# Kernel optimization log

Measured on AMD Instinct MI355X. Metric: run time of the kernel, lower is better.

The kernel has to match this reference:

```python
import jax, jax.numpy as jnp
import numpy as np

L = 2            # layer_num
NNEI = 120       # neighbors
ED = 64          # embed_dim
HD = 128         # hidden_dim
B = 4096         # nframes * nloc
SCALING = HD ** (-0.5)
LN_EPS = 1e-5


def _l2norm(x):
    # torch F.normalize: x / max(||x||, 1e-12)
    n = jnp.sqrt(jnp.sum(x * x, axis=-1, keepdims=True))
    return x / jnp.maximum(n, 1e-12)


def setup_inputs() -> dict:
    key = jax.random.key(0)
    ks = jax.random.split(key, 10)
    input_G = jax.random.normal(ks[0], (B, NNEI, ED), dtype=jnp.float32)
    nei_mask = jax.random.randint(ks[1], (B, NNEI), 0, 2) > 0
    nei_mask = nei_mask.at[:, 0].set(True)  # ensure >=1 valid neighbor (avoid all -inf rows)
    r = jax.random.normal(ks[2], (B, NNEI, 3), dtype=jnp.float32)
    input_r = _l2norm(r)  # normalized radial
    std_in = 1.0 / np.sqrt(3 * HD + ED)
    std_out = 1.0 / np.sqrt(ED + HD)
    in_w = jax.random.normal(ks[3], (L, ED, 3 * HD), dtype=jnp.float32) * std_in
    in_b = jax.random.normal(ks[4], (L, 3 * HD), dtype=jnp.float32)
    out_w = jax.random.normal(ks[5], (L, HD, ED), dtype=jnp.float32) * std_out
    out_b = jax.random.normal(ks[6], (L, ED), dtype=jnp.float32)
    ln_g = jnp.ones((L, ED), dtype=jnp.float32)
    ln_b = jnp.zeros((L, ED), dtype=jnp.float32)
    return {"input_G": input_G, "nei_mask": nei_mask, "input_r": input_r,
            "in_w": in_w, "in_b": in_b, "out_w": out_w, "out_b": out_b,
            "ln_g": ln_g, "ln_b": ln_b}


def _layer_norm(x, g, b):
    mu = jnp.mean(x, axis=-1, keepdims=True)
    var = jnp.mean((x - mu) ** 2, axis=-1, keepdims=True)
    return (x - mu) * jax.lax.rsqrt(var + LN_EPS) * g + b


def reference(input_G, nei_mask, input_r, in_w, in_b, out_w, out_b, ln_g, ln_b):
    # angular gate: [B, nnei, nnei]
    ang = jnp.einsum('bnd,bmd->bnm', input_r, input_r)
    mask_k = nei_mask[:, None, :]   # mask over keys
    mask_q = nei_mask[:, :, None]   # mask over queries
    x = input_G
    for l in range(L):
        residual = x
        qkv = jnp.einsum('bne,ef->bnf', x, in_w[l]) + in_b[l]
        q, k, v = jnp.split(qkv, 3, axis=-1)           # each [B, nnei, HD]
        q = _l2norm(q) * SCALING
        k = _l2norm(k)
        v = _l2norm(v)
        aw = jnp.einsum('bnh,bmh->bnm', q, k)
        aw = jnp.where(mask_k, aw, -jnp.inf)
        aw = jax.nn.softmax(aw, axis=-1)
        aw = jnp.where(mask_q, aw, 0.0)
        aw = aw * ang                                   # dotr angular gating
        o = jnp.einsum('bnm,bmh->bnh', aw, v)
        x = residual + jnp.einsum('bnh,he->bne', o, out_w[l]) + out_b[l]
        x = _layer_norm(x, ln_g[l], ln_b[l])            # post_ln
    return x
```

## Files before the change

kernel.cpp:

```cpp
#include <hip/hip_runtime.h>
#include <math.h>

#define LAYERS 2
#define NNEI 120
#define NPAD 128
#define ED 64
#define HD 128
#define NB 4096
#define F3 (3*HD)
#define SCALING 0.088388347648318447f
#define LN_EPS 1e-5f
#define T 512
#define XP 72
#define QPAD 136

typedef unsigned short u16;
typedef unsigned int u32;
typedef unsigned char u8;
typedef float f32x4 __attribute__((ext_vector_type(4)));
typedef short bf16x8 __attribute__((ext_vector_type(8)));

__device__ __forceinline__ float bf2f(u16 u) { return __uint_as_float(((u32)u) << 16); }
__device__ __forceinline__ u16 f2bf(float f) {
  u32 i = __float_as_uint(f);
  u32 r = (i + 0x7fffu + ((i >> 16) & 1u)) >> 16;
  return (u16)r;
}
__device__ __forceinline__ float gldr(const void* p, long i, bool f32) {
  return f32 ? ((const float*)p)[i] : bf2f(((const u16*)p)[i]);
}

__device__ __forceinline__ float red16sum(float v) {
  v += __shfl_xor(v, 1); v += __shfl_xor(v, 2);
  v += __shfl_xor(v, 4); v += __shfl_xor(v, 8);
  return v;
}
__device__ __forceinline__ float red16max(float v) {
  v = fmaxf(v, __shfl_xor(v, 1)); v = fmaxf(v, __shfl_xor(v, 2));
  v = fmaxf(v, __shfl_xor(v, 4)); v = fmaxf(v, __shfl_xor(v, 8));
  return v;
}

#define MFMA(a, b, d) (d) = __builtin_amdgcn_mfma_f32_16x16x32_bf16((a), (b), (d), 0, 0, 0)

__device__ __forceinline__ void gload_lds16(const u16* src, u16* dst) {
  __builtin_amdgcn_global_load_lds(
      (const __attribute__((address_space(1))) u32*)(const void*)src,
      (__attribute__((address_space(3))) u32*)(void*)dst, 16, 0, 0);
}

__device__ __forceinline__ void stage16(const u16* __restrict__ hi, const u16* __restrict__ lo,
                                        long base, int kstride, u16* sbuf, int wave, int lane) {
  #pragma unroll
  for (int kk = 0; kk < 2; ++kk) {
    const int i = 2 * wave + kk;
    const int col = 4 * i + (lane >> 4);
    const int slot = lane & 15;
    const int chunk = (slot & 7) ^ (col & 7);
    const u16* src = ((slot < 8) ? hi : lo) + base + (long)col * kstride + 8 * chunk;
    gload_lds16(src, sbuf + i * 512);
  }
}

__device__ __forceinline__ bf16x8 rdfrag(const u16* sbuf, int col, int chunk, int c7, int lo) {
  const int slot = (chunk ^ c7) + (lo << 3);
  return *(const bf16x8*)(sbuf + col * 128 + slot * 8);
}

__global__ void detect_kernel(const u16* __restrict__ G,
                              const u8* __restrict__ mask,
                              int* __restrict__ flags) {
  __shared__ int sf[2];
  const int t = threadIdx.x;
  if (t < 2) sf[t] = 0;
  __syncthreads();
  int isf = 0;
  for (int i = t; i < 256; i += 256) {
    int e = (G[2 * i] >> 7) & 0xff;
    if (e >= 150) isf = 1;
  }
  int mb = 0;
  for (int i = t; i < 4096; i += 256) {
    if (i && (i & 3) && mask[i]) mb = 1;
  }
  if (isf) atomicOr(&sf[0], 1);
  if (mb) atomicOr(&sf[1], 1);
  __syncthreads();
  if (t < 2) flags[t] = sf[t];
}

__global__ void prep_kernel(const void* __restrict__ in_w, const void* __restrict__ out_w,
                            u16* __restrict__ wt_hi, u16* __restrict__ wt_lo,
                            u16* __restrict__ ow_hi, u16* __restrict__ ow_lo,
                            const int* __restrict__ flags) {
  const bool f32 = flags[0] != 0;
  const int i = blockIdx.x * blockDim.x + threadIdx.x;
  if (i < LAYERS * F3 * ED) {
    const int l = i / (F3 * ED);
    const int rem = i % (F3 * ED);
    const int f = rem / ED;
    const int e = rem % ED;
    const long src = (long)(l * ED + e) * F3 + f;
    const float w = f32 ? ((const float*)in_w)[src] : bf2f(((const u16*)in_w)[src]);
    const u16 h = f2bf(w);
    wt_hi[i] = h;
    wt_lo[i] = f2bf(w - bf2f(h));
  }
  if (i < LAYERS * ED * HD) {
    const int l = i / (ED * HD);
    const int rem = i % (ED * HD);
    const int e = rem / HD;
    const int hh = rem % HD;
    const long src = (long)(l * HD + hh) * ED + e;
    const float w = f32 ? ((const float*)out_w)[src] : bf2f(((const u16*)out_w)[src]);
    const u16 h = f2bf(w);
    ow_hi[i] = h;
    ow_lo[i] = f2bf(w - bf2f(h));
  }
}

__global__ __launch_bounds__(T, 2) void nwa_kernel(
    const void* __restrict__ G, const void* __restrict__ mask,
    const void* __restrict__ rr,
    const void* __restrict__ in_b, const void* __restrict__ out_b,
    const void* __restrict__ ln_g, const void* __restrict__ ln_b,
    const u16* __restrict__ wt_hi, const u16* __restrict__ wt_lo,
    const u16* __restrict__ ow_hi, const u16* __restrict__ ow_lo,
    void* __restrict__ out, const int* __restrict__ flags)
{
  const bool f32f = flags[0] != 0;
  const bool mbyte = flags[1] != 0;

  __shared__ __align__(16) u16 x_hi[NPAD][XP];
  __shared__ __align__(16) u16 x_lo[NPAD][XP];
  __shared__ __align__(16) u16 q_s[NPAD][QPAD];
  __shared__ __align__(16) u16 k_s[NPAD][QPAD];
  __shared__ __align__(16) u16 vT_s[HD][QPAD];
  __shared__ __align__(16) float r_s[NPAD][4];
  __shared__ int m_s[NPAD];

  const int b = blockIdx.x;
  const int t = threadIdx.x;
  const int wave = t >> 6;
  const int lane = t & 63;
  const int g = lane >> 4;
  const int c = lane & 15;
  const int c7 = c & 7;
  u16* sbase = &q_s[0][0];

  {
    const long gbase = (long)b * (NNEI * ED);
    for (int i = t; i < NNEI * ED; i += T) {
      const int rrow = i >> 6, cc = i & 63;
      if (f32f) {
        const float v = ((const float*)G)[gbase + i];
        const u16 h = f2bf(v);
        x_hi[rrow][cc] = h;
        x_lo[rrow][cc] = f2bf(v - bf2f(h));
      } else {
        x_hi[rrow][cc] = ((const u16*)G)[gbase + i];
        x_lo[rrow][cc] = 0;
      }
    }
    for (int i = t; i < (NPAD - NNEI) * ED; i += T) {
      x_hi[NNEI + (i >> 6)][i & 63] = 0;
      x_lo[NNEI + (i >> 6)][i & 63] = 0;
    }
    const long rbase = (long)b * (NNEI * 3);
    const long mbase = (long)b * NNEI;
    for (int i = t; i < NPAD; i += T) {
      if (i < NNEI) {
        r_s[i][0] = gldr(rr, rbase + i * 3 + 0, f32f);
        r_s[i][1] = gldr(rr, rbase + i * 3 + 1, f32f);
        r_s[i][2] = gldr(rr, rbase + i * 3 + 2, f32f);
        r_s[i][3] = 0.f;
        m_s[i] = mbyte ? (int)((const u8*)mask)[mbase + i] : ((const int*)mask)[mbase + i];
      } else {
        r_s[i][0] = 0.f; r_s[i][1] = 0.f; r_s[i][2] = 0.f; r_s[i][3] = 0.f;
        m_s[i] = 0;
      }
    }
  }
  __syncthreads();

  int vmask = 0;
  #pragma unroll
  for (int mt = 0; mt < 8; ++mt) vmask |= (m_s[16 * mt + c] ? 1 : 0) << mt;
  float qmr[4];
  #pragma unroll
  for (int r = 0; r < 4; ++r) qmr[r] = m_s[16 * wave + 4 * g + r] ? 1.f : 0.f;

  for (int l = 0; l < LAYERS; ++l) {
    const long wofs = (long)l * (F3 * ED);
    const long bbase = (long)l * F3;
    const long oofs = (long)l * (ED * HD);

    bf16x8 a_hi[2], a_lo[2];
    #pragma unroll
    for (int kf = 0; kf < 2; ++kf) {
      a_hi[kf] = *(const bf16x8*)&x_hi[16 * wave + c][32 * kf + 8 * g];
      a_lo[kf] = *(const bf16x8*)&x_lo[16 * wave + c][32 * kf + 8 * g];
    }
    f32x4 accQ[8], accB[8];
    #pragma unroll
    for (int i2 = 0; i2 < 8; ++i2) { accQ[i2] = (f32x4){0,0,0,0}; accB[i2] = (f32x4){0,0,0,0}; }

    stage16(wt_hi, wt_lo, wofs + (long)2 * 64 * 64, 64, sbase, wave, lane);
    __syncthreads();

    #pragma unroll
    for (int ss = 0; ss < 6; ++ss) {
      const int n = (ss + 2) % 6;
      if (ss < 5) {
        const int nn = (ss + 3) % 6;
        stage16(wt_hi, wt_lo, wofs + (long)nn * 64 * 64, 64,
                sbase + ((ss + 1) & 1) * 8192, wave, lane);
      }
      const u16* sb = sbase + (ss & 1) * 8192;
      const bool isQ = (n < 2);
      #pragma unroll
      for (int ct = 0; ct < 4; ++ct) {
        const int tt = 4 * n + ct;
        const int nt = tt & 7;
        const int col = 16 * ct + c;
        const bf16x8 bh0 = rdfrag(sb, col, g, c7, 0);
        const bf16x8 bh1 = rdfrag(sb, col, 4 + g, c7, 0);
        const bf16x8 bl0 = rdfrag(sb, col, g, c7, 1);
        const bf16x8 bl1 = rdfrag(sb, col, 4 + g, c7, 1);
        f32x4 d = isQ ? accQ[nt] : accB[nt];
        MFMA(a_hi[0], bh0, d); MFMA(a_hi[1], bh1, d);
        MFMA(a_lo[0], bh0, d); MFMA(a_lo[1], bh1, d);
        MFMA(a_hi[0], bl0, d); MFMA(a_hi[1], bl1, d);
        if (isQ) accQ[nt] = d; else accB[nt] = d;
      }
      if (ss == 1) {
        float invr[4];
        #pragma unroll
        for (int nt = 0; nt < 8; ++nt) {
          const float bias = gldr(in_b, bbase + 128 + 16 * nt + c, f32f);
          accB[nt][0] += bias; accB[nt][1] += bias; accB[nt][2] += bias; accB[nt][3] += bias;
        }
        #pragma unroll
        for (int r = 0; r < 4; ++r) {
          float ssum = 0.f;
          #pragma unroll
          for (int nt = 0; nt < 8; ++nt) ssum += accB[nt][r] * accB[nt][r];
          ssum = red16sum(ssum);
          invr[r] = 1.f / fmaxf(sqrtf(ssum), 1e-12f);
        }
        #pragma unroll
        for (int nt = 0; nt < 8; ++nt) {
          #pragma unroll
          for (int r = 0; r < 4; ++r)
            k_s[16 * wave + 4 * g + r][16 * nt + c] = f2bf(accB[nt][r] * invr[r]);
          accB[nt] = (f32x4){0,0,0,0};
        }
      } else if (ss == 3) {
        float invr[4];
        #pragma unroll
        for (int nt = 0; nt < 8; ++nt) {
          const float bias = gldr(in_b, bbase + 256 + 16 * nt + c, f32f);
          accB[nt][0] += bias; accB[nt][1] += bias; accB[nt][2] += bias; accB[nt][3] += bias;
        }
        #pragma unroll
        for (int r = 0; r < 4; ++r) {
          float ssum = 0.f;
          #pragma unroll
          for (int nt = 0; nt < 8; ++nt) ssum += accB[nt][r] * accB[nt][r];
          ssum = red16sum(ssum);
          invr[r] = 1.f / fmaxf(sqrtf(ssum), 1e-12f);
        }
        #pragma unroll
        for (int nt = 0; nt < 8; ++nt) {
          const u32 p01 = (u32)f2bf(accB[nt][0] * invr[0]) | ((u32)f2bf(accB[nt][1] * invr[1]) << 16);
          const u32 p23 = (u32)f2bf(accB[nt][2] * invr[2]) | ((u32)f2bf(accB[nt][3] * invr[3]) << 16);
          *(u32*)&vT_s[16 * nt + c][16 * wave + 4 * g + 0] = p01;
          *(u32*)&vT_s[16 * nt + c][16 * wave + 4 * g + 2] = p23;
        }
      }
      __syncthreads();
    }
    {
      float invr[4];
      #pragma unroll
      for (int nt = 0; nt < 8; ++nt) {
        const float bias = gldr(in_b, bbase + 16 * nt + c, f32f);
        accQ[nt][0] += bias; accQ[nt][1] += bias; accQ[nt][2] += bias; accQ[nt][3] += bias;
      }
      #pragma unroll
      for (int r = 0; r < 4; ++r) {
        float ssum = 0.f;
        #pragma unroll
        for (int nt = 0; nt < 8; ++nt) ssum += accQ[nt][r] * accQ[nt][r];
        ssum = red16sum(ssum);
        invr[r] = SCALING / fmaxf(sqrtf(ssum), 1e-12f);
      }
      #pragma unroll
      for (int nt = 0; nt < 8; ++nt)
        #pragma unroll
        for (int r = 0; r < 4; ++r)
          q_s[16 * wave + 4 * g + r][16 * nt + c] = f2bf(accQ[nt][r] * invr[r]);
    }

    f32x4 s[8];
    {
      bf16x8 aq[4];
      #pragma unroll
      for (int kf = 0; kf < 4; ++kf)
        aq[kf] = *(const bf16x8*)&q_s[16 * wave + c][32 * kf + 8 * g];
      #pragma unroll
      for (int mt = 0; mt < 8; ++mt) {
        const u16* kp = &k_s[16 * mt + c][8 * g];
        f32x4 d = {0.f, 0.f, 0.f, 0.f};
        #pragma unroll
        for (int kf = 0; kf < 4; ++kf)
          MFMA(aq[kf], *(const bf16x8*)(kp + 32 * kf), d);
        s[mt] = d;
      }
    }

    {
      const f32x4 minf = {-INFINITY, -INFINITY, -INFINITY, -INFINITY};
      #pragma unroll
      for (int mt = 0; mt < 8; ++mt)
        if (!((vmask >> mt) & 1)) s[mt] = minf;
      float inv[4];
      float4 rnr[4];
      #pragma unroll
      for (int r = 0; r < 4; ++r) {
        float mx = s[0][r];
        #pragma unroll
        for (int mt = 1; mt < 8; ++mt) mx = fmaxf(mx, s[mt][r]);
        mx = red16max(mx);
        float sm = 0.f;
        #pragma unroll
        for (int mt = 0; mt < 8; ++mt) {
          const float e = __expf(s[mt][r] - mx);
          s[mt][r] = e;
          sm += e;
        }
        sm = red16sum(sm);
        inv[r] = qmr[r] / sm;
        rnr[r] = *(const float4*)&r_s[16 * wave + 4 * g + r][0];
      }
      #pragma unroll
      for (int mt = 0; mt < 8; ++mt) {
        const float4 rm = *(const float4*)&r_s[16 * mt + c][0];
        #pragma unroll
        for (int r = 0; r < 4; ++r) {
          const float w = s[mt][r] * inv[r] *
              (rnr[r].x * rm.x + rnr[r].y * rm.y + rnr[r].z * rm.z);
          q_s[16 * wave + 4 * g + r][16 * mt + c] = f2bf(w);
        }
      }
    }

    {
      bf16x8 pa[4];
      #pragma unroll
      for (int kf = 0; kf < 4; ++kf)
        pa[kf] = *(const bf16x8*)&q_s[16 * wave + c][32 * kf + 8 * g];
      f32x4 o[8];
      #pragma unroll
      for (int ht = 0; ht < 8; ++ht) {
        const u16* vp = &vT_s[16 * ht + c][8 * g];
        f32x4 d = {0.f, 0.f, 0.f, 0.f};
        #pragma unroll
        for (int kf = 0; kf < 4; ++kf)
          MFMA(pa[kf], *(const bf16x8*)(vp + 32 * kf), d);
        o[ht] = d;
      }
      #pragma unroll
      for (int ht = 0; ht < 8; ++ht)
        #pragma unroll
        for (int r = 0; r < 4; ++r)
          q_s[16 * wave + 4 * g + r][16 * ht + c] = f2bf(o[ht][r]);
    }

    bf16x8 ao[4];
    #pragma unroll
    for (int kf = 0; kf < 4; ++kf)
      ao[kf] = *(const bf16x8*)&q_s[16 * wave + c][32 * kf + 8 * g];
    __syncthreads();
    stage16(ow_hi, ow_lo, oofs, 128, sbase, wave, lane);
    __syncthreads();
    f32x4 dv[4];
    #pragma unroll
    for (int nt = 0; nt < 4; ++nt) dv[nt] = (f32x4){0,0,0,0};
    #pragma unroll
    for (int kh = 0; kh < 2; ++kh) {
      if (kh == 0) stage16(ow_hi, ow_lo, oofs + 64, 128, sbase + 8192, wave, lane);
      const u16* sb = sbase + kh * 8192;
      #pragma unroll
      for (int nt = 0; nt < 4; ++nt) {
        const int col = 16 * nt + c;
        #pragma unroll
        for (int kfl = 0; kfl < 2; ++kfl) {
          const bf16x8 bh = rdfrag(sb, col, 4 * kfl + g, c7, 0);
          const bf16x8 bl = rdfrag(sb, col, 4 * kfl + g, c7, 1);
          f32x4 d2 = dv[nt];
          MFMA(ao[2 * kh + kfl], bh, d2);
          MFMA(ao[2 * kh + kfl], bl, d2);
          dv[nt] = d2;
        }
      }
      if (kh == 0) __syncthreads();
    }
    {
      float gg[4], bbv[4];
      #pragma unroll
      for (int nt = 0; nt < 4; ++nt) {
        const int e = 16 * nt + c;
        const float ob = gldr(out_b, (long)l * ED + e, f32f);
        gg[nt]  = gldr(ln_g, (long)l * ED + e, f32f);
        bbv[nt] = gldr(ln_b, (long)l * ED + e, f32f);
        #pragma unroll
        for (int r = 0; r < 4; ++r) {
          const int n = 16 * wave + 4 * g + r;
          dv[nt][r] += ob + bf2f(x_hi[n][e]) + bf2f(x_lo[n][e]);
        }
      }
      #pragma unroll
      for (int r = 0; r < 4; ++r) {
        const int n = 16 * wave + 4 * g + r;
        float mu = dv[0][r] + dv[1][r] + dv[2][r] + dv[3][r];
        mu = red16sum(mu) * (1.f / 64.f);
        float var = 0.f;
        #pragma unroll
        for (int nt = 0; nt < 4; ++nt) { const float dd = dv[nt][r] - mu; var += dd * dd; }
        var = red16sum(var) * (1.f / 64.f);
        const float rs = rsqrtf(var + LN_EPS);
        if (n < NNEI) {
          #pragma unroll
          for (int nt = 0; nt < 4; ++nt) {
            const float y = (dv[nt][r] - mu) * rs * gg[nt] + bbv[nt];
            const u16 hh = f2bf(y);
            x_hi[n][16 * nt + c] = hh;
            x_lo[n][16 * nt + c] = f2bf(y - bf2f(hh));
            if (l == LAYERS - 1) {
              const long oidx = (long)b * (NNEI * ED) + (long)n * ED + 16 * nt + c;
              if (f32f) ((float*)out)[oidx] = y;
              else      ((u16*)out)[oidx] = f2bf(y);
            }
          }
        }
      }
    }
  }
}

extern "C" void kernel_launch(void* const* d_in, const int* in_sizes, int n_in,
                              void* d_out, int out_size, void* d_ws, size_t ws_size,
                              hipStream_t stream) {
  (void)in_sizes; (void)n_in; (void)out_size; (void)ws_size;
  const void* G = d_in[0];
  const void* mask = d_in[1];
  const void* rr = d_in[2];
  const void* in_w = d_in[3];
  const void* in_b = d_in[4];
  const void* out_w = d_in[5];
  const void* out_b = d_in[6];
  const void* ln_g = d_in[7];
  const void* ln_b = d_in[8];

  int* flags = (int*)d_ws;
  u16* wt_hi = (u16*)((char*)d_ws + 256);
  u16* wt_lo = wt_hi + LAYERS * F3 * ED;
  u16* ow_hi = wt_lo + LAYERS * F3 * ED;
  u16* ow_lo = ow_hi + LAYERS * ED * HD;

  detect_kernel<<<dim3(1), dim3(256), 0, stream>>>((const u16*)G, (const u8*)mask, flags);
  prep_kernel<<<dim3(96), dim3(T), 0, stream>>>(in_w, out_w, wt_hi, wt_lo, ow_hi, ow_lo, flags);
  nwa_kernel<<<dim3(NB), dim3(T), 0, stream>>>(
      G, mask, rr, in_b, out_b, ln_g, ln_b, wt_hi, wt_lo, ow_hi, ow_lo, d_out, flags);
}
```

Baseline: 897.1 us.

## Split each 16-row band across two waves with 1024-thread blocks

Doubles the block to 16 waves so each 16-row band is split across two waves, each handling half of the output columns. Row norms, softmax sums and LayerNorm statistics become cross-wave reductions through small shared buffers, with extra barriers. The softmax drops its max subtraction, which is safe only because the scores are bounded by normalised q and k. Also skips the lo-part MFMAs when the input is bf16 in layer 0, prefetches the next layer's weights early, and uses a hardware bf16 conversion. The cost is more synchronisation per block and possibly fewer resident blocks per CU.

Measured after the change: 847.0 us. 1.06x faster.

```diff
diff --git a/kernel.cpp b/kernel.cpp
--- a/kernel.cpp
+++ b/kernel.cpp
@@ -10,7 +10,7 @@
 #define F3 (3*HD)
 #define SCALING 0.088388347648318447f
 #define LN_EPS 1e-5f
-#define T 512
+#define T 1024
 #define XP 72
 #define QPAD 136
 
@@ -22,24 +22,20 @@
 
 __device__ __forceinline__ float bf2f(u16 u) { return __uint_as_float(((u32)u) << 16); }
 __device__ __forceinline__ u16 f2bf(float f) {
-  u32 i = __float_as_uint(f);
-  u32 r = (i + 0x7fffu + ((i >> 16) & 1u)) >> 16;
-  return (u16)r;
+  __bf16 b = (__bf16)f;
+  return __builtin_bit_cast(u16, b);
+}
+__device__ __forceinline__ u32 pk2bf(float lo, float hi) {
+  return (u32)f2bf(lo) | ((u32)f2bf(hi) << 16);
 }
 __device__ __forceinline__ float gldr(const void* p, long i, bool f32) {
   return f32 ? ((const float*)p)[i] : bf2f(((const u16*)p)[i]);
 }
-
 __device__ __forceinline__ float red16sum(float v) {
   v += __shfl_xor(v, 1); v += __shfl_xor(v, 2);
   v += __shfl_xor(v, 4); v += __shfl_xor(v, 8);
   return v;
 }
-__device__ __forceinline__ float red16max(float v) {
-  v = fmaxf(v, __shfl_xor(v, 1)); v = fmaxf(v, __shfl_xor(v, 2));
-  v = fmaxf(v, __shfl_xor(v, 4)); v = fmaxf(v, __shfl_xor(v, 8));
-  return v;
-}
 
 #define MFMA(a, b, d) (d) = __builtin_amdgcn_mfma_f32_16x16x32_bf16((a), (b), (d), 0, 0, 0)
 
@@ -51,15 +47,11 @@
 
 __device__ __forceinline__ void stage16(const u16* __restrict__ hi, const u16* __restrict__ lo,
                                         long base, int kstride, u16* sbuf, int wave, int lane) {
-  #pragma unroll
-  for (int kk = 0; kk < 2; ++kk) {
-    const int i = 2 * wave + kk;
-    const int col = 4 * i + (lane >> 4);
-    const int slot = lane & 15;
-    const int chunk = (slot & 7) ^ (col & 7);
-    const u16* src = ((slot < 8) ? hi : lo) + base + (long)col * kstride + 8 * chunk;
-    gload_lds16(src, sbuf + i * 512);
-  }
+  const int col = 4 * wave + (lane >> 4);
+  const int slot = lane & 15;
+  const int chunk = (slot & 7) ^ (col & 7);
+  const u16* src = ((slot < 8) ? hi : lo) + base + (long)col * kstride + 8 * chunk;
+  gload_lds16(src, sbuf + wave * 512);
 }
 
 __device__ __forceinline__ bf16x8 rdfrag(const u16* sbuf, int col, int chunk, int c7, int lo) {
@@ -119,7 +111,7 @@
   }
 }
 
-__global__ __launch_bounds__(T, 2) void nwa_kernel(
+__global__ __launch_bounds__(T) void nwa_kernel(
     const void* __restrict__ G, const void* __restrict__ mask,
     const void* __restrict__ rr,
     const void* __restrict__ in_b, const void* __restrict__ out_b,
@@ -137,11 +129,15 @@
   __shared__ __align__(16) u16 k_s[NPAD][QPAD];
   __shared__ __align__(16) u16 vT_s[HD][QPAD];
   __shared__ __align__(16) float r_s[NPAD][4];
+  __shared__ __align__(16) float pA[2][8][16];
+  __shared__ __align__(16) float pB[2][8][16];
   __shared__ int m_s[NPAD];
 
   const int b = blockIdx.x;
   const int t = threadIdx.x;
   const int wave = t >> 6;
+  const int band = wave & 7;
+  const int half = wave >> 3;
   const int lane = t & 63;
   const int g = lane >> 4;
   const int c = lane & 15;
@@ -181,264 +177,275 @@
       }
     }
   }
+  stage16(wt_hi, wt_lo, (long)2 * 4096, 64, sbase, wave, lane);
   __syncthreads();
 
-  int vmask = 0;
+  int vm[4];
   #pragma unroll
-  for (int mt = 0; mt < 8; ++mt) vmask |= (m_s[16 * mt + c] ? 1 : 0) << mt;
+  for (int mtl = 0; mtl < 4; ++mtl) vm[mtl] = m_s[16 * (4 * half + mtl) + c];
   float qmr[4];
   #pragma unroll
-  for (int r = 0; r < 4; ++r) qmr[r] = m_s[16 * wave + 4 * g + r] ? 1.f : 0.f;
+  for (int r = 0; r < 4; ++r) qmr[r] = m_s[16 * band + 4 * g + r] ? 1.f : 0.f;
 
   for (int l = 0; l < LAYERS; ++l) {
     const long wofs = (long)l * (F3 * ED);
     const long bbase = (long)l * F3;
     const long oofs = (long)l * (ED * HD);
+    const bool use_lo = f32f || (l > 0);
 
     bf16x8 a_hi[2], a_lo[2];
     #pragma unroll
     for (int kf = 0; kf < 2; ++kf) {
-      a_hi[kf] = *(const bf16x8*)&x_hi[16 * wave + c][32 * kf + 8 * g];
-      a_lo[kf] = *(const bf16x8*)&x_lo[16 * wave + c][32 * kf + 8 * g];
-    }
-    f32x4 accQ[8], accB[8];
+      a_hi[kf] = *(const bf16x8*)&x_hi[16 * band + c][32 * kf + 8 * g];
+      a_lo[kf] = *(const bf16x8*)&x_lo[16 * band + c][32 * kf + 8 * g];
+    }
+    f32x4 accQ[4], accB[4];
     #pragma unroll
-    for (int i2 = 0; i2 < 8; ++i2) { accQ[i2] = (f32x4){0,0,0,0}; accB[i2] = (f32x4){0,0,0,0}; }
-
-    stage16(wt_hi, wt_lo, wofs + (long)2 * 64 * 64, 64, sbase, wave, lane);
-    __syncthreads();
+    for (int j = 0; j < 4; ++j) { accQ[j] = (f32x4){0,0,0,0}; accB[j] = (f32x4){0,0,0,0}; }
 
     #pragma unroll
     for (int ss = 0; ss < 6; ++ss) {
       const int n = (ss + 2) % 6;
-      if (ss < 5) {
-        const int nn = (ss + 3) % 6;
-        stage16(wt_hi, wt_lo, wofs + (long)nn * 64 * 64, 64,
+      if (ss < 5)
+        stage16(wt_hi, wt_lo, wofs + (long)((ss + 3) % 6) * 4096, 64,
                 sbase + ((ss + 1) & 1) * 8192, wave, lane);
+      if (ss == 2) {
+        const f32x4 sa = *(const f32x4*)&pA[0][band][4 * g];
+        const f32x4 sb4 = *(const f32x4*)&pA[1][band][4 * g];
+        float invr[4];
+        #pragma unroll
+        for (int r = 0; r < 4; ++r) invr[r] = rsqrtf(fmaxf(sa[r] + sb4[r], 1e-24f));
+        #pragma unroll
+        for (int j = 0; j < 4; ++j) {
+          const int nt = 4 * (j >> 1) + 2 * half + (j & 1);
+          #pragma unroll
+          for (int r = 0; r < 4; ++r)
+            k_s[16 * band + 4 * g + r][16 * nt + c] = f2bf(accB[j][r] * invr[r]);
+          accB[j] = (f32x4){0,0,0,0};
+        }
+      }
+      if (ss == 4) {
+        const f32x4 sa = *(const f32x4*)&pB[0][band][4 * g];
+        const f32x4 sb4 = *(const f32x4*)&pB[1][band][4 * g];
+        float invr[4];
+        #pragma unroll
+        for (int r = 0; r < 4; ++r) invr[r] = rsqrtf(fmaxf(sa[r] + sb4[r], 1e-24f));
+        #pragma unroll
+        for (int j = 0; j < 4; ++j) {
+          const int nt = 4 * (j >> 1) + 2 * half + (j & 1);
+          const u32 p01 = pk2bf(accB[j][0] * invr[0], accB[j][1] * invr[1]);
+          const u32 p23 = pk2bf(accB[j][2] * invr[2], accB[j][3] * invr[3]);
+          *(u32*)&vT_s[16 * nt + c][16 * band + 4 * g + 0] = p01;
+          *(u32*)&vT_s[16 * nt + c][16 * band + 4 * g + 2] = p23;
+        }
       }
       const u16* sb = sbase + (ss & 1) * 8192;
-      const bool isQ = (n < 2);
-      #pragma unroll
-      for (int ct = 0; ct < 4; ++ct) {
-        const int tt = 4 * n + ct;
-        const int nt = tt & 7;
-        const int col = 16 * ct + c;
+      #pragma unroll
+      for (int ctl = 0; ctl < 2; ++ctl) {
+        const int col = 16 * (2 * half + ctl) + c;
+        const int j = 2 * (n & 1) + ctl;
         const bf16x8 bh0 = rdfrag(sb, col, g, c7, 0);
         const bf16x8 bh1 = rdfrag(sb, col, 4 + g, c7, 0);
         const bf16x8 bl0 = rdfrag(sb, col, g, c7, 1);
         const bf16x8 bl1 = rdfrag(sb, col, 4 + g, c7, 1);
-        f32x4 d = isQ ? accQ[nt] : accB[nt];
+        f32x4 d = (n < 2) ? accQ[j] : accB[j];
         MFMA(a_hi[0], bh0, d); MFMA(a_hi[1], bh1, d);
-        MFMA(a_lo[0], bh0, d); MFMA(a_lo[1], bh1, d);
+        if (use_lo) { MFMA(a_lo[0], bh0, d); MFMA(a_lo[1], bh1, d); }
         MFMA(a_hi[0], bl0, d); MFMA(a_hi[1], bl1, d);
-        if (isQ) accQ[nt] = d; else accB[nt] = d;
-      }
-      if (ss == 1) {
-        float invr[4];
-        #pragma unroll
-        for (int nt = 0; nt < 8; ++nt) {
-          const float bias = gldr(in_b, bbase + 128 + 16 * nt + c, f32f);
-          accB[nt][0] += bias; accB[nt][1] += bias; accB[nt][2] += bias; accB[nt][3] += bias;
-        }
+        if (n < 2) accQ[j] = d; else accB[j] = d;
+      }
+      if (ss == 1 || ss == 3 || ss == 5) {
+        const int fo = (ss == 1) ? 128 : (ss == 3) ? 256 : 0;
+        f32x4* acc = (ss == 5) ? accQ : accB;
+        #pragma unroll
+        for (int j = 0; j < 4; ++j) {
+          const int nt = 4 * (j >> 1) + 2 * half + (j & 1);
+          const float bias = gldr(in_b, bbase + fo + 16 * nt + c, f32f);
+          acc[j][0] += bias; acc[j][1] += bias; acc[j][2] += bias; acc[j][3] += bias;
+        }
+        float* dst = (ss == 3) ? &pB[half][band][0] : &pA[half][band][0];
         #pragma unroll
         for (int r = 0; r < 4; ++r) {
-          float ssum = 0.f;
-          #pragma unroll
-          for (int nt = 0; nt < 8; ++nt) ssum += accB[nt][r] * accB[nt][r];
-          ssum = red16sum(ssum);
-          invr[r] = 1.f / fmaxf(sqrtf(ssum), 1e-12f);
-        }
-        #pragma unroll
-        for (int nt = 0; nt < 8; ++nt) {
-          #pragma unroll
-          for (int r = 0; r < 4; ++r)
-            k_s[16 * wave + 4 * g + r][16 * nt + c] = f2bf(accB[nt][r] * invr[r]);
-          accB[nt] = (f32x4){0,0,0,0};
-        }
-      } else if (ss == 3) {
-        float invr[4];
-        #pragma unroll
-        for (int nt = 0; nt < 8; ++nt) {
-          const float bias = gldr(in_b, bbase + 256 + 16 * nt + c, f32f);
-          accB[nt][0] += bias; accB[nt][1] += bias; accB[nt][2] += bias; accB[nt][3] += bias;
-        }
-        #pragma unroll
-        for (int r = 0; r < 4; ++r) {
-          float ssum = 0.f;
-          #pragma unroll
-          for (int nt = 0; nt < 8; ++nt) ssum += accB[nt][r] * accB[nt][r];
-          ssum = red16sum(ssum);
-          invr[r] = 1.f / fmaxf(sqrtf(ssum), 1e-12f);
-        }
-        #pragma unroll
-        for (int nt = 0; nt < 8; ++nt) {
-          const u32 p01 = (u32)f2bf(accB[nt][0] * invr[0]) | ((u32)f2bf(accB[nt][1] * invr[1]) << 16);
-          const u32 p23 = (u32)f2bf(accB[nt][2] * invr[2]) | ((u32)f2bf(accB[nt][3] * invr[3]) << 16);
-          *(u32*)&vT_s[16 * nt + c][16 * wave + 4 * g + 0] = p01;
-          *(u32*)&vT_s[16 * nt + c][16 * wave + 4 * g + 2] = p23;
+          const float ssum = acc[0][r] * acc[0][r] + acc[1][r] * acc[1][r] +
+                             acc[2][r] * acc[2][r] + acc[3][r] * acc[3][r];
+          const float red = red16sum(ssum);
+          if (c == 0) dst[4 * g + r] = red;
         }
       }
       __syncthreads();
     }
     {
+      const f32x4 sa = *(const f32x4*)&pA[0][band][4 * g];
+      const f32x4 sb4 = *(const f32x4*)&pA[1][band][4 * g];
       float invr[4];
       #pragma unroll
-      for (int nt = 0; nt < 8; ++nt) {
-        const float bias = gldr(in_b, bbase + 16 * nt + c, f32f);
-        accQ[nt][0] += bias; accQ[nt][1] += bias; accQ[nt][2] += bias; accQ[nt][3] += bias;
-      }
-      #pragma unroll
-      for (int r = 0; r < 4; ++r) {
-        float ssum = 0.f;
-        #pragma unroll
-        for (int nt = 0; nt < 8; ++nt) ssum += accQ[nt][r] * accQ[nt][r];
-        ssum = red16sum(ssum);
-        invr[r] = SCALING / fmaxf(sqrtf(ssum), 1e-12f);
-      }
-      #pragma unroll
-      for (int nt = 0; nt < 8; ++nt)
+      for (int r = 0; r < 4; ++r) invr[r] = SCALING * rsqrtf(fmaxf(sa[r] + sb4[r], 1e-24f));
+      #pragma unroll
+      for (int j = 0; j < 4; ++j) {
+        const int nt = 4 * (j >> 1) + 2 * half + (j & 1);
         #pragma unroll
         for (int r = 0; r < 4; ++r)
-          q_s[16 * wave + 4 * g + r][16 * nt + c] = f2bf(accQ[nt][r] * invr[r]);
-    }
-
-    f32x4 s[8];
+          q_s[16 * band + 4 * g + r][16 * nt + c] = f2bf(accQ[j][r] * invr[r]);
+      }
+    }
+    __syncthreads();
+
+    f32x4 s4[4];
     {
       bf16x8 aq[4];
       #pragma unroll
       for (int kf = 0; kf < 4; ++kf)
-        aq[kf] = *(const bf16x8*)&q_s[16 * wave + c][32 * kf + 8 * g];
-      #pragma unroll
-      for (int mt = 0; mt < 8; ++mt) {
-        const u16* kp = &k_s[16 * mt + c][8 * g];
+        aq[kf] = *(const bf16x8*)&q_s[16 * band + c][32 * kf + 8 * g];
+      #pragma unroll
+      for (int mtl = 0; mtl < 4; ++mtl) {
+        const u16* kp = &k_s[16 * (4 * half + mtl) + c][8 * g];
         f32x4 d = {0.f, 0.f, 0.f, 0.f};
         #pragma unroll
         for (int kf = 0; kf < 4; ++kf)
           MFMA(aq[kf], *(const bf16x8*)(kp + 32 * kf), d);
-        s[mt] = d;
-      }
-    }
-
-    {
-      const f32x4 minf = {-INFINITY, -INFINITY, -INFINITY, -INFINITY};
-      #pragma unroll
-      for (int mt = 0; mt < 8; ++mt)
-        if (!((vmask >> mt) & 1)) s[mt] = minf;
+        s4[mtl] = d;
+      }
+    }
+    {
+      float psum[4] = {0.f, 0.f, 0.f, 0.f};
+      #pragma unroll
+      for (int mtl = 0; mtl < 4; ++mtl) {
+        #pragma unroll
+        for (int r = 0; r < 4; ++r) {
+          const float e = vm[mtl] ? __expf(s4[mtl][r]) : 0.f;
+          s4[mtl][r] = e;
+          psum[r] += e;
+        }
+      }
+      #pragma unroll
+      for (int r = 0; r < 4; ++r) {
+        const float red = red16sum(psum[r]);
+        if (c == 0) pA[half][band][4 * g + r] = red;
+      }
+    }
+    __syncthreads();
+    {
+      const f32x4 sa = *(const f32x4*)&pA[0][band][4 * g];
+      const f32x4 sb4 = *(const f32x4*)&pA[1][band][4 * g];
       float inv[4];
-      float4 rnr[4];
+      f32x4 rn[4];
       #pragma unroll
       for (int r = 0; r < 4; ++r) {
-        float mx = s[0][r];
-        #pragma unroll
-        for (int mt = 1; mt < 8; ++mt) mx = fmaxf(mx, s[mt][r]);
-        mx = red16max(mx);
-        float sm = 0.f;
-        #pragma unroll
-        for (int mt = 0; mt < 8; ++mt) {
-          const float e = __expf(s[mt][r] - mx);
-          s[mt][r] = e;
-          sm += e;
-        }
-        sm = red16sum(sm);
-        inv[r] = qmr[r] / sm;
-        rnr[r] = *(const float4*)&r_s[16 * wave + 4 * g + r][0];
-      }
-      #pragma unroll
-      for (int mt = 0; mt < 8; ++mt) {
-        const float4 rm = *(const float4*)&r_s[16 * mt + c][0];
+        inv[r] = qmr[r] / (sa[r] + sb4[r]);
+        rn[r] = *(const f32x4*)&r_s[16 * band + 4 * g + r][0];
+      }
+      #pragma unroll
+      for (int mtl = 0; mtl < 4; ++mtl) {
+        const int mt = 4 * half + mtl;
+        const f32x4 rm = *(const f32x4*)&r_s[16 * mt + c][0];
         #pragma unroll
         for (int r = 0; r < 4; ++r) {
-          const float w = s[mt][r] * inv[r] *
-              (rnr[r].x * rm.x + rnr[r].y * rm.y + rnr[r].z * rm.z);
-          q_s[16 * wave + 4 * g + r][16 * mt + c] = f2bf(w);
-        }
-      }
-    }
+          const float w = s4[mtl][r] * inv[r] *
+              (rn[r][0] * rm[0] + rn[r][1] * rm[1] + rn[r][2] * rm[2]);
+          q_s[16 * band + 4 * g + r][16 * mt + c] = f2bf(w);
+        }
+      }
+    }
+    __syncthreads();
 
     {
       bf16x8 pa[4];
       #pragma unroll
       for (int kf = 0; kf < 4; ++kf)
-        pa[kf] = *(const bf16x8*)&q_s[16 * wave + c][32 * kf + 8 * g];
-      f32x4 o[8];
-      #pragma unroll
-      for (int ht = 0; ht < 8; ++ht) {
-        const u16* vp = &vT_s[16 * ht + c][8 * g];
+        pa[kf] = *(const bf16x8*)&q_s[16 * band + c][32 * kf + 8 * g];
+      f32x4 o4[4];
+      #pragma unroll
+      for (int htl = 0; htl < 4; ++htl) {
+        const u16* vp = &vT_s[16 * (4 * half + htl) + c][8 * g];
         f32x4 d = {0.f, 0.f, 0.f, 0.f};
         #pragma unroll
         for (int kf = 0; kf < 4; ++kf)
           MFMA(pa[kf], *(const bf16x8*)(vp + 32 * kf), d);
-        o[ht] = d;
-      }
-      #pragma unroll
-      for (int ht = 0; ht < 8; ++ht)
+        o4[htl] = d;
+      }
+      #pragma unroll
+      for (int htl = 0; htl < 4; ++htl)
         #pragma unroll
         for (int r = 0; r < 4; ++r)
-          q_s[16 * wave + 4 * g + r][16 * ht + c] = f2bf(o[ht][r]);
-    }
+          k_s[16 * band + 4 * g + r][16 * (4 * half + htl) + c] = f2bf(o4[htl][r]);
+    }
+    __syncthreads();
 
     bf16x8 ao[4];
     #pragma unroll
     for (int kf = 0; kf < 4; ++kf)
-      ao[kf] = *(const bf16x8*)&q_s[16 * wave + c][32 * kf + 8 * g];
-    __syncthreads();
+      ao[kf] = *(const bf16x8*)&k_s[16 * band + c][32 * kf + 8 * g];
     stage16(ow_hi, ow_lo, oofs, 128, sbase, wave, lane);
     __syncthreads();
-    f32x4 dv[4];
-    #pragma unroll
-    for (int nt = 0; nt < 4; ++nt) dv[nt] = (f32x4){0,0,0,0};
+    f32x4 dv[2];
+    dv[0] = (f32x4){0,0,0,0}; dv[1] = (f32x4){0,0,0,0};
     #pragma unroll
     for (int kh = 0; kh < 2; ++kh) {
       if (kh == 0) stage16(ow_hi, ow_lo, oofs + 64, 128, sbase + 8192, wave, lane);
       const u16* sb = sbase + kh * 8192;
       #pragma unroll
-      for (int nt = 0; nt < 4; ++nt) {
-        const int col = 16 * nt + c;
+      for (int ntl = 0; ntl < 2; ++ntl) {
+        const int col = 16 * (2 * half + ntl) + c;
         #pragma unroll
         for (int kfl = 0; kfl < 2; ++kfl) {
           const bf16x8 bh = rdfrag(sb, col, 4 * kfl + g, c7, 0);
           const bf16x8 bl = rdfrag(sb, col, 4 * kfl + g, c7, 1);
-          f32x4 d2 = dv[nt];
-          MFMA(ao[2 * kh + kfl], bh, d2);
-          MFMA(ao[2 * kh + kfl], bl, d2);
-          dv[nt] = d2;
+          MFMA(ao[2 * kh + kfl], bh, dv[ntl]);
+          MFMA(ao[2 * kh + kfl], bl, dv[ntl]);
         }
       }
       if (kh == 0) __syncthreads();
     }
-    {
-      float gg[4], bbv[4];
-      #pragma unroll
-      for (int nt = 0; nt < 4; ++nt) {
-        const int e = 16 * nt + c;
-        const float ob = gldr(out_b, (long)l * ED + e, f32f);
-        gg[nt]  = gldr(ln_g, (long)l * ED + e, f32f);
-        bbv[nt] = gldr(ln_b, (long)l * ED + e, f32f);
+    if (l + 1 < LAYERS)
+      stage16(wt_hi, wt_lo, (long)(l + 1) * (F3 * ED) + (long)2 * 4096, 64, sbase, wave, lane);
+    {
+      #pragma unroll
+      for (int ntl = 0; ntl < 2; ++ntl) {
+        const int e0 = 16 * (2 * half + ntl) + c;
+        const float ob = gldr(out_b, (long)l * ED + e0, f32f);
         #pragma unroll
         for (int r = 0; r < 4; ++r) {
-          const int n = 16 * wave + 4 * g + r;
-          dv[nt][r] += ob + bf2f(x_hi[n][e]) + bf2f(x_lo[n][e]);
+          const int nrow = 16 * band + 4 * g + r;
+          dv[ntl][r] += ob + bf2f(x_hi[nrow][e0]) + bf2f(x_lo[nrow][e0]);
         }
       }
       #pragma unroll
       for (int r = 0; r < 4; ++r) {
-        const int n = 16 * wave + 4 * g + r;
-        float mu = dv[0][r] + dv[1][r] + dv[2][r] + dv[3][r];
-        mu = red16sum(mu) * (1.f / 64.f);
-        float var = 0.f;
-        #pragma unroll
-        for (int nt = 0; nt < 4; ++nt) { const float dd = dv[nt][r] - mu; var += dd * dd; }
-        var = red16sum(var) * (1.f / 64.f);
-        const float rs = rsqrtf(var + LN_EPS);
-        if (n < NNEI) {
+        const float sx = red16sum(dv[0][r] + dv[1][r]);
+        const float sxx = red16sum(dv[0][r] * dv[0][r] + dv[1][r] * dv[1][r]);
+        if (c == 0) { pA[half][band][4 * g + r] = sx; pB[half][band][4 * g + r] = sxx; }
+      }
+    }
+    __syncthreads();
+    {
+      const f32x4 xa = *(const f32x4*)&pA[0][band][4 * g];
+      const f32x4 xb = *(const f32x4*)&pA[1][band][4 * g];
+      const f32x4 ya = *(const f32x4*)&pB[0][band][4 * g];
+      const f32x4 yb = *(const f32x4*)&pB[1][band][4 * g];
+      float gg[2], bbv[2];
+      #pragma unroll
+      for (int ntl = 0; ntl < 2; ++ntl) {
+        const int e0 = 16 * (2 * half + ntl) + c;
+        gg[ntl]  = gldr(ln_g, (long)l * ED + e0, f32f);
+        bbv[ntl] = gldr(ln_b, (long)l * ED + e0, f32f);
+      }
+      #pragma unroll
+      for (int r = 0; r < 4; ++r) {
+        const int nrow = 16 * band + 4 * g + r;
+        const float mu = (xa[r] + xb[r]) * (1.f / 64.f);
+        const float ex2 = (ya[r] + yb[r]) * (1.f / 64.f);
+        const float rs = rsqrtf(fmaxf(ex2 - mu * mu, 0.f) + LN_EPS);
+        if (nrow < NNEI) {
           #pragma unroll
-          for (int nt = 0; nt < 4; ++nt) {
-            const float y = (dv[nt][r] - mu) * rs * gg[nt] + bbv[nt];
-            const u16 hh = f2bf(y);
-            x_hi[n][16 * nt + c] = hh;
-            x_lo[n][16 * nt + c] = f2bf(y - bf2f(hh));
-            if (l == LAYERS - 1) {
-              const long oidx = (long)b * (NNEI * ED) + (long)n * ED + 16 * nt + c;
+          for (int ntl = 0; ntl < 2; ++ntl) {
+            const int e0 = 16 * (2 * half + ntl) + c;
+            const float y = (dv[ntl][r] - mu) * rs * gg[ntl] + bbv[ntl];
+            if (l + 1 < LAYERS) {
+              const u16 hh2 = f2bf(y);
+              x_hi[nrow][e0] = hh2;
+              x_lo[nrow][e0] = f2bf(y - bf2f(hh2));
+            } else {
+              const long oidx = (long)b * (NNEI * ED) + (long)nrow * ED + e0;
               if (f32f) ((float*)out)[oidx] = y;
               else      ((u16*)out)[oidx] = f2bf(y);
             }
@@ -446,6 +453,7 @@
         }
       }
     }
+    if (l + 1 < LAYERS) __syncthreads();
   }
 }
 
@@ -470,7 +478,7 @@
   u16* ow_lo = ow_hi + LAYERS * ED * HD;
 
   detect_kernel<<<dim3(1), dim3(256), 0, stream>>>((const u16*)G, (const u8*)mask, flags);
-  prep_kernel<<<dim3(96), dim3(T), 0, stream>>>(in_w, out_w, wt_hi, wt_lo, ow_hi, ow_lo, flags);
+  prep_kernel<<<dim3(96), dim3(512), 0, stream>>>(in_w, out_w, wt_hi, wt_lo, ow_hi, ow_lo, flags);
   nwa_kernel<<<dim3(NB), dim3(T), 0, stream>>>(
       G, mask, rr, in_b, out_b, ln_g, ln_b, wt_hi, wt_lo, ow_hi, ow_lo, d_out, flags);
 }
```
